# Optimization experiments

Measured on AMD Instinct MI355X. Metric: run time of the kernel, lower is better.

Reference implementation:

```python
import jax, jax.numpy as jnp
import numpy as np

N_ENTITY = 8000
N_REL = 100
N_GROUPS = 64
HIDDEN = 256
D_MODEL = 256
N_LAYERS = 2
N_HEADS = 4
GP = 64          # group_proj_dim
GH = 2           # group attn heads
D_TOTAL = D_MODEL * N_LAYERS
D_FEAT = D_TOTAL + 2 * HIDDEN
B, L = 16, 512


def time_enc(t, d):
    # sinusoidal temporal encoding: [..., d]
    i = jnp.arange(d // 2)
    freqs = jnp.exp(-jnp.log(10000.0) * (2.0 * i / d)).astype(t.dtype)
    ang = t[..., None] * freqs
    return jnp.concatenate([jnp.sin(ang), jnp.cos(ang)], axis=-1)


def layer_norm(x, w, b, eps=1e-5):
    mu = jnp.mean(x, axis=-1, keepdims=True)
    var = jnp.mean((x - mu) ** 2, axis=-1, keepdims=True)
    return (x - mu) / jnp.sqrt(var + eps) * w + b


def mh_attn(q, k, v, n_heads, mask=None):
    Bq, Lq, E = q.shape
    hd = E // n_heads
    qh = q.reshape(Bq, Lq, n_heads, hd)
    kh = k.reshape(Bq, -1, n_heads, hd)
    vh = v.reshape(Bq, -1, n_heads, hd)
    s = jnp.einsum('bqhd,bkhd->bhqk', qh, kh) / np.sqrt(hd).astype(np.float32)
    if mask is not None:
        s = jnp.where(mask, s, jnp.asarray(-1e9, s.dtype))
    a = jax.nn.softmax(s, axis=-1)
    return jnp.einsum('bhqk,bkhd->bqhd', a, vh).reshape(Bq, Lq, E)


def setup_inputs() -> dict:
    key = jax.random.key(0)
    ks = iter(jax.random.split(key, 48))
    w = lambda *s: jax.random.normal(next(ks), s, jnp.float32) * 0.02
    inp = {}
    inp['subs'] = jax.random.randint(next(ks), (B, L), 0, N_ENTITY)
    inp['marks'] = jax.random.randint(next(ks), (B, L), 0, N_REL)
    inp['objs'] = jax.random.randint(next(ks), (B, L), 0, N_ENTITY)
    inp['times'] = jax.random.uniform(next(ks), (B, L), jnp.float32)
    inp['dt'] = jax.random.uniform(next(ks), (B, L), jnp.float32)
    inp['mask'] = jax.random.randint(next(ks), (B, L), 0, 2).astype(bool)
    inp['group_map'] = jax.random.randint(next(ks), (N_ENTITY * N_REL,), 0, N_GROUPS)
    # AttNHP core params
    inp['obj_embed'] = w(N_ENTITY, D_MODEL)
    inp['core_Wq'] = w(N_LAYERS, D_MODEL, D_MODEL)
    inp['core_Wk'] = w(N_LAYERS, D_MODEL, D_MODEL)
    inp['core_Wv'] = w(N_LAYERS, D_MODEL, D_MODEL)
    inp['core_Wo'] = w(N_LAYERS, D_MODEL, D_MODEL)
    # GAttNHP params
    inp['sub_embed'] = w(N_ENTITY, HIDDEN)
    inp['rel_embed'] = w(N_REL, HIDDEN)
    inp['gp_w'] = w(D_FEAT, GP)
    inp['gp_b'] = jnp.zeros((GP,), jnp.float32)
    inp['ga_in_w'] = w(GP, 3 * GP)
    inp['ga_in_b'] = jnp.zeros((3 * GP,), jnp.float32)
    inp['ga_out_w'] = w(GP, GP)
    inp['ga_out_b'] = jnp.zeros((GP,), jnp.float32)
    inp['ffn_w1'] = w(GP, GP)
    inp['ffn_b1'] = jnp.zeros((GP,), jnp.float32)
    inp['ffn_w2'] = w(GP, GP)
    inp['ffn_b2'] = jnp.zeros((GP,), jnp.float32)
    inp['n1_w'] = jnp.ones((GP,), jnp.float32)
    inp['n1_b'] = jnp.zeros((GP,), jnp.float32)
    inp['n2_w'] = jnp.ones((GP,), jnp.float32)
    inp['n2_b'] = jnp.zeros((GP,), jnp.float32)
    inp['mg_w'] = w(D_FEAT + GP, D_FEAT)
    inp['mg_b'] = jnp.zeros((D_FEAT,), jnp.float32)
    inp['int_w'] = w(D_FEAT, N_ENTITY)
    inp['int_b'] = jnp.zeros((N_ENTITY,), jnp.float32)
    return inp


def reference(subs, marks, objs, times, dt, mask, group_map,
              obj_embed, core_Wq, core_Wk, core_Wv, core_Wo,
              sub_embed, rel_embed, gp_w, gp_b, ga_in_w, ga_in_b,
              ga_out_w, ga_out_b, ffn_w1, ffn_b1, ffn_w2, ffn_b2,
              n1_w, n1_b, n2_w, n2_b, mg_w, mg_b, int_w, int_b):
    Bb, Ll = objs.shape
    Lh = Ll - 1
    # ---- AttNHP core (forward_along_seqs) ----
    hist = objs[:, :-1]
    x = obj_embed[hist] + time_enc(times[:, :-1], D_MODEL) + time_enc(dt[:, :-1], D_MODEL)
    cur = time_enc(times[:, 1:], D_MODEL)                       # queries at query_times
    causal = jnp.tril(jnp.ones((Lh, Lh), bool))[None, None]     # [1,1,Lq,Lk]
    layer_outs = []
    for l in range(N_LAYERS):
        q = cur @ core_Wq[l]
        k = x @ core_Wk[l]
        v = x @ core_Wv[l]
        cur = cur + mh_attn(q, k, v, N_HEADS, causal) @ core_Wo[l]
        layer_outs.append(cur)
    enc_out = jnp.concatenate(layer_outs, axis=-1)              # [B,Lh,D_TOTAL]
    # ---- base features ----
    s_emb = jnp.broadcast_to(sub_embed[subs[:, 0]][:, None, :], (Bb, Lh, HIDDEN))
    r_emb = jnp.broadcast_to(rel_embed[marks[:, 0]][:, None, :], (Bb, Lh, HIDDEN))
    feats = jnp.concatenate([enc_out, s_emb, r_emb], axis=-1)   # [B,Lh,D_FEAT]
    # ---- group interaction: scatter-mean -> attn+ffn -> gather -> merge ----
    g_ids = group_map[subs * N_REL + marks][:, :-1]             # [B,Lh]
    flat_f = feats.reshape(-1, D_FEAT)
    fm = mask[:, :-1].reshape(-1).astype(flat_f.dtype)          # float validity mask
    keys = jnp.repeat(jnp.arange(Bb), Lh) * N_GROUPS + g_ids.reshape(-1)
    nseg = Bb * N_GROUPS
    gsum = jax.ops.segment_sum(flat_f * fm[:, None], keys, num_segments=nseg)
    gcnt = jax.ops.segment_sum(fm, keys, num_segments=nseg)
    rep = (gsum / jnp.maximum(gcnt, 1.0)[:, None]).reshape(Bb, N_GROUPS, D_FEAT)
    gp = rep @ gp_w + gp_b                                      # [B,G,64]
    qg, kg, vg = jnp.split(gp @ ga_in_w + ga_in_b, 3, axis=-1)
    ga = mh_attn(qg, kg, vg, GH) @ ga_out_w + ga_out_b
    gn = layer_norm(gp + ga, n1_w, n1_b)
    ff = jax.nn.relu(gn @ ffn_w1 + ffn_b1) @ ffn_w2 + ffn_b2
    gout = layer_norm(gn + ff, n2_w, n2_b)                      # [B,G,64]
    gathered = gout.reshape(-1, GP)[keys] * fm[:, None]         # zeros where invalid
    merged = jnp.concatenate([flat_f, gathered], axis=-1)
    enhanced = (merged @ mg_w + mg_b).reshape(Bb, Lh, D_FEAT)
    # ---- intensity head ----
    return jax.nn.softplus(enhanced @ int_w + int_b)            # [B,Lh,N_ENTITY]
```

## Files before the change

### kernel.cpp

```cpp
#include <hip/hip_runtime.h>
#include <hip/hip_bf16.h>
#include <cstdint>
#include <cstddef>

#define B_    16
#define L_    512
#define LH    511
#define RTOT  (B_*LH)
#define DM    256
#define DFEAT 1024
#define NG    64
#define GPDIM 64
#define NENT  8000
#define NRELS 100
#define RS    8000
#define RS2   16000

#define COL_X     0
#define COL_CUR   256
#define COL_Q     512
#define COL_K     768
#define COL_V     1024
#define COL_ATTN  1280
#define COL_FF    1536
#define COL_GATH  2560
#define COL_GSUM  3000
#define COL_GCNT  4100
#define COL_GP    4200
#define COL_GOUT  4300
#define COL_FLAG  5000
#define BCOL_ENCW 5248
#define BCOL_MGWT 11104
#define BCOL_MGA  12192
#define BCOL_WT   13824
#define BCOL_ENH  14848
#define N1        6912

#define WS_OFF_K  2228224ull
#define WS_OFF_V  (WS_OFF_K + 4186112ull)
#define WS_NEED2  (WS_OFF_V + 4194304ull)
#define WS2_BT    0ull
#define WS2_ENH   2359296ull
#define WS2_K     WS2_ENH
#define WS2_V     (WS2_K + 4186112ull)
#define WS_NEED3  (WS2_ENH + 16744448ull)

static constexpr float LN1E4_OVER_128 = 0.07195578415606394f;

typedef __attribute__((ext_vector_type(8))) short short8;
typedef __attribute__((ext_vector_type(4))) short sshort4;
typedef __attribute__((ext_vector_type(4))) float f32x4;
typedef __attribute__((ext_vector_type(2))) float f32x2;

__device__ __forceinline__ short bf16b(float x){
  union { __hip_bfloat16 h; short s; } u; u.h = __float2bfloat16(x); return u.s;
}

__device__ __forceinline__ float fast_softplus(float v) {
  return fmaxf(v, 0.f) + __logf(1.0f + __expf(-fabsf(v)));
}

__device__ __forceinline__ void gload16(const void* g, void* l) {
  __builtin_amdgcn_global_load_lds(
      (const __attribute__((address_space(1))) unsigned int*)g,
      (__attribute__((address_space(3))) unsigned int*)l, 16, 0, 0);
}

__global__ __launch_bounds__(256) void k_detect(const unsigned int* __restrict__ m,
                                                float* __restrict__ outbuf) {
  __shared__ int bad;
  if (threadIdx.x == 0) bad = 0;
  __syncthreads();
  int local = 0;
  for (int i = threadIdx.x; i < 2048; i += 256)
    if (m[i] > 1u) local = 1;
  if (local) bad = 1;
  __syncthreads();
  if (threadIdx.x == 0) ((int*)outbuf)[COL_FLAG] = bad;
}

__device__ __forceinline__ int mask_at(const void* m, int idx, int boolmode) {
  return boolmode ? (int)((const unsigned char*)m)[idx] : ((const int*)m)[idx];
}

__global__ __launch_bounds__(256) void k_build_x_cur(
    const int* __restrict__ objs, const float* __restrict__ times,
    const float* __restrict__ dts, const float* __restrict__ obj_embed,
    float* __restrict__ out)
{
  int bt = blockIdx.x;
  int b = bt / LH, t = bt - b * LH;
  int d = threadIdx.x;
  int i = d & 127;
  float freq = expf(-(float)i * LN1E4_OVER_128);
  float t0 = times[b*L_ + t];
  float t1 = times[b*L_ + t + 1];
  float dtv = dts[b*L_ + t];
  float a0 = t0*freq, ad = dtv*freq, a1 = t1*freq;
  bool lo = (d < 128);
  float te0 = lo ? sinf(a0) : cosf(a0);
  float ted = lo ? sinf(ad) : cosf(ad);
  float te1 = lo ? sinf(a1) : cosf(a1);
  int obj = objs[b*L_ + t];
  out[(size_t)bt*RS + COL_X   + d] = obj_embed[(size_t)obj*DM + d] + te0 + ted;
  out[(size_t)bt*RS + COL_CUR + d] = te1;
}

template<bool AF32, int EPI>
__global__ __launch_bounds__(256) void gemm_mfma(
    const void* __restrict__ Aptr, long strideA,
    const short* __restrict__ Bt, long strideB,
    const float* __restrict__ bias,
    float* __restrict__ Cf, long strideC,
    __hip_bfloat16* __restrict__ Cb, long strideCb,
    float* __restrict__ aux, long ldaux, int auxoff,
    int M, int K)
{
  int lane = threadIdx.x & 63;
  int wid  = threadIdx.x >> 6;
  int wm = wid >> 1, wn = wid & 1;
  int r15 = lane & 15, koct = lane >> 4;
  int m0 = blockIdx.y*128 + wm*64;
  int n0 = blockIdx.x*128 + wn*64;
  f32x4 acc[4][4] = {};
  int ar[4];
  #pragma unroll
  for (int mf = 0; mf < 4; ++mf) {
    int r = m0 + mf*16 + r15;
    ar[mf] = r < M ? r : M-1;
  }
  const short* Ab = (const short*)Aptr;
  const float* Af = (const float*)Aptr;
  for (int k0 = 0; k0 < K; k0 += 32) {
    int kk = k0 + koct*8;
    short8 a[4], b[4];
    #pragma unroll
    for (int mf = 0; mf < 4; ++mf) {
      if (AF32) {
        const float* p = Af + (size_t)ar[mf]*strideA + kk;
        f32x4 lo = *(const f32x4*)p;
        f32x4 hi = *(const f32x4*)(p + 4);
        short8 t;
        #pragma unroll
        for (int i = 0; i < 4; ++i) { t[i] = bf16b(lo[i]); t[i+4] = bf16b(hi[i]); }
        a[mf] = t;
      } else {
        a[mf] = *(const short8*)(Ab + (size_t)ar[mf]*strideA + kk);
      }
    }
    #pragma unroll
    for (int nf = 0; nf < 4; ++nf) {
      int n = n0 + nf*16 + r15;
      b[nf] = *(const short8*)(Bt + (size_t)n*strideB + kk);
    }
    #pragma unroll
    for (int mf = 0; mf < 4; ++mf)
      #pragma unroll
      for (int nf = 0; nf < 4; ++nf)
        acc[mf][nf] = __builtin_amdgcn_mfma_f32_16x16x32_bf16(a[mf], b[nf], acc[mf][nf], 0, 0, 0);
  }
  #pragma unroll
  for (int mf = 0; mf < 4; ++mf) {
    #pragma unroll
    for (int r = 0; r < 4; ++r) {
      int grow = m0 + mf*16 + koct*4 + r;
      if (grow >= M) continue;
      #pragma unroll
      for (int nf = 0; nf < 4; ++nf) {
        int gcol = n0 + nf*16 + r15;
        float v = acc[mf][nf][r];
        size_t ci = (size_t)grow*strideC + gcol;
        if (EPI == 2) {
          v += Cf[ci];
          Cf[ci] = v;
          aux[(size_t)grow*ldaux + auxoff + gcol] = v;
        } else {
          Cf[ci] = v;
        }
      }
    }
  }
}

template<int EPI>
__global__ __launch_bounds__(256) void gemm_mfma_lds(
    const short* __restrict__ A, long strideA,
    const short* __restrict__ Bt, long strideB,
    const float* __restrict__ bias,
    float* __restrict__ Cf, long strideC,
    __hip_bfloat16* __restrict__ Cb, long strideCb,
    __hip_bfloat16* __restrict__ Cb2, long strideCb2,
    int M, int N, int K)
{
  __shared__ short8 sA[128][8];
  __shared__ short8 sB[128][8];
  int tid = threadIdx.x;
  int lane = tid & 63;
  int w = tid >> 6;
  int wm = w >> 1, wn = w & 1;
  int r15 = lane & 15, koct = lane >> 4;

  int gx = gridDim.x;
  int nwg = gx * gridDim.y;
  int bid = blockIdx.y * gx + blockIdx.x;
  int bx, by;
  if (gridDim.y == 64 && (nwg & 7) == 0) {
    int xcd = bid & 7, c = bid >> 3;
    by = xcd*8 + (c & 7);
    bx = c >> 3;
  } else {
    bx = blockIdx.x; by = blockIdx.y;
  }
  int m0 = by * 128, n0 = bx * 128;

  const short* aSrc[4]; const short* bSrc[4];
  {
    int row = w*32 + (lane >> 3);
    int slot = lane & 7;
    #pragma unroll
    for (int c = 0; c < 4; ++c) {
      int r = row + c*8;
      int ga = m0 + r; if (ga > M-1) ga = M-1;
      int gb = n0 + r;
      int sw = slot ^ (r & 7);
      aSrc[c] = A  + (size_t)ga*strideA + sw*8;
      bSrc[c] = Bt + (size_t)gb*strideB + sw*8;
    }
  }

  f32x4 acc[4][4] = {};
  for (int k0 = 0; k0 < K; k0 += 64) {
    #pragma unroll
    for (int c = 0; c < 4; ++c) {
      gload16(aSrc[c] + k0, (short8*)sA + (w*4 + c)*64);
      gload16(bSrc[c] + k0, (short8*)sB + (w*4 + c)*64);
    }
    __syncthreads();
    #pragma unroll
    for (int ks = 0; ks < 2; ++ks) {
      short8 a[4], b[4];
      #pragma unroll
      for (int mf = 0; mf < 4; ++mf) {
        int lr = wm*64 + mf*16 + r15;
        a[mf] = sA[lr][(ks*4 + koct) ^ (lr & 7)];
      }
      #pragma unroll
      for (int nf = 0; nf < 4; ++nf) {
        int lr = wn*64 + nf*16 + r15;
        b[nf] = sB[lr][(ks*4 + koct) ^ (lr & 7)];
      }
      #pragma unroll
      for (int mf = 0; mf < 4; ++mf)
        #pragma unroll
        for (int nf = 0; nf < 4; ++nf)
          acc[mf][nf] = __builtin_amdgcn_mfma_f32_16x16x32_bf16(a[mf], b[nf], acc[mf][nf], 0, 0, 0);
    }
    __syncthreads();
  }
  #pragma unroll
  for (int mf = 0; mf < 4; ++mf) {
    #pragma unroll
    for (int r = 0; r < 4; ++r) {
      int grow = m0 + wm*64 + mf*16 + koct*4 + r;
      if (grow >= M) continue;
      #pragma unroll
      for (int nf = 0; nf < 4; ++nf) {
        int gcol = n0 + wn*64 + nf*16 + r15;
        if (gcol >= N) continue;
        float v = acc[mf][nf][r] + bias[gcol];
        if (EPI == 0) {
          __builtin_nontemporal_store(fast_softplus(v), &Cf[(size_t)grow*strideC + gcol]);
        } else {
          __hip_bfloat16 hb = __float2bfloat16(v);
          Cb[(size_t)grow*strideCb + gcol] = hb;
          if (Cb2) Cb2[(size_t)grow*strideCb2 + gcol] = hb;
        }
      }
    }
  }
}

__global__ __launch_bounds__(256) void k_transpose_bf16(
    const float* __restrict__ W, int ldw,
    __hip_bfloat16* __restrict__ Wt, long strideT)
{
  __shared__ float s[64][65];
  int n0 = blockIdx.x * 64, k0 = blockIdx.y * 64;
  int tid = threadIdx.x;
  for (int p = 0; p < 16; ++p) {
    int idx = p*256 + tid;
    int kk = idx >> 6, nn = idx & 63;
    s[kk][nn] = W[(size_t)(k0+kk)*ldw + n0 + nn];
  }
  __syncthreads();
  for (int p = 0; p < 16; ++p) {
    int idx = p*256 + tid;
    int nn = idx >> 6, kk = idx & 63;
    Wt[(size_t)(n0+nn)*strideT + k0 + kk] = __float2bfloat16(s[kk][nn]);
  }
}

__global__ __launch_bounds__(256) void k_castA(float* __restrict__ out)
{
  int r = blockIdx.x;
  int tid = threadIdx.x;
  const float* src = out + (size_t)r*RS + COL_FF;
  short* dst = (short*)out + (size_t)r*RS2 + BCOL_MGA;
  for (int i = tid; i < 1088; i += 256)
    dst[i] = bf16b(src[i]);
}

__global__ __launch_bounds__(256) void k_kvcast(
    const float* __restrict__ out, short* __restrict__ Kb, short* __restrict__ Vt)
{
  __shared__ float sV[32][65];
  int tt = blockIdx.x, bh = blockIdx.y;
  int b = bh >> 2, h = bh & 3;
  int tid = threadIdx.x;
  #pragma unroll
  for (int i = 0; i < 8; ++i) {
    int idx = i*256 + tid;
    int tp = idx >> 6, d = idx & 63;
    int t = tt*32 + tp;
    float vv = 0.f;
    if (t < LH) {
      const float* row = out + (size_t)(b*LH + t)*RS;
      Kb[((size_t)bh*511 + t)*64 + d] = bf16b(row[COL_K + h*64 + d]);
      vv = row[COL_V + h*64 + d];
    }
    sV[tp][d] = vv;
  }
  __syncthreads();
  #pragma unroll
  for (int i = 0; i < 8; ++i) {
    int idx = i*256 + tid;
    int d = idx >> 5, tp = idx & 31;
    Vt[((size_t)bh*64 + d)*512 + tt*32 + tp] = bf16b(sV[tp][d]);
  }
}

__global__ __launch_bounds__(64) void k_attn_mfma(float* __restrict__ out)
{
  int qt = blockIdx.x, h = blockIdx.y, b = blockIdx.z;
  int lane = threadIdx.x & 63;
  int r15 = lane & 15, koct = lane >> 4;
  __shared__ short Vt[64][40];
  __shared__ short Pl[16][40];
  const float* base = out + (size_t)b*LH*RS;

  int qrow = qt*16 + r15; if (qrow > LH-1) qrow = LH-1;
  const float* qp = base + (size_t)qrow*RS + COL_Q + h*64 + koct*8;
  short8 qf[2];
  #pragma unroll
  for (int d2 = 0; d2 < 2; ++d2) {
    f32x4 lo = *(const f32x4*)(qp + d2*32);
    f32x4 hi = *(const f32x4*)(qp + d2*32 + 4);
    short8 t;
    #pragma unroll
    for (int i = 0; i < 4; ++i) { t[i] = bf16b(lo[i]); t[i+4] = bf16b(hi[i]); }
    qf[d2] = t;
  }

  f32x4 o[4] = {};
  float m = -3.0e38f, l = 0.f;
  int qg = qt*16 + r15;
  int nt = qt/2 + 1;

  for (int ti = 0; ti < nt; ++ti) {
    int kv0 = ti*32;
    __syncthreads();
    {
      const float* vbase = base + COL_V + h*64 + lane;
      #pragma unroll 4
      for (int j = 0; j < 32; ++j) {
        int kvr = kv0 + j; if (kvr > LH-1) kvr = LH-1;
        Vt[lane][j] = bf16b(vbase[(size_t)kvr*RS]);
      }
    }
    f32x4 s[2] = {};
    #pragma unroll
    for (int kvf = 0; kvf < 2; ++kvf) {
      int kvr = kv0 + kvf*16 + r15; if (kvr > LH-1) kvr = LH-1;
      const float* kp = base + (size_t)kvr*RS + COL_K + h*64 + koct*8;
      #pragma unroll
      for (int d2 = 0; d2 < 2; ++d2) {
        f32x4 lo = *(const f32x4*)(kp + d2*32);
        f32x4 hi = *(const f32x4*)(kp + d2*32 + 4);
        short8 t;
        #pragma unroll
        for (int i = 0; i < 4; ++i) { t[i] = bf16b(lo[i]); t[i+4] = bf16b(hi[i]); }
        s[kvf] = __builtin_amdgcn_mfma_f32_16x16x32_bf16(t, qf[d2], s[kvf], 0, 0, 0);
      }
    }
    float sv[2][4];
    float mx = -3.0e38f;
    #pragma unroll
    for (int kvf = 0; kvf < 2; ++kvf)
      #pragma unroll
      for (int r = 0; r < 4; ++r) {
        int kvg = kv0 + kvf*16 + koct*4 + r;
        float x = s[kvf][r] * 0.125f;
        if (kvg > qg) x = -3.0e38f;
        sv[kvf][r] = x;
        mx = fmaxf(mx, x);
      }
    mx = fmaxf(mx, __shfl_xor(mx, 16));
    mx = fmaxf(mx, __shfl_xor(mx, 32));
    float mn = fmaxf(m, mx);
    float alpha = expf(m - mn);
    m = mn;
    float ls = 0.f;
    sshort4 pk[2];
    #pragma unroll
    for (int kvf = 0; kvf < 2; ++kvf)
      #pragma unroll
      for (int r = 0; r < 4; ++r) {
        float p = expf(sv[kvf][r] - mn);
        ls += p;
        pk[kvf][r] = bf16b(p);
      }
    l = l*alpha + ls;
    *(sshort4*)&Pl[r15][koct*4]      = pk[0];
    *(sshort4*)&Pl[r15][16 + koct*4] = pk[1];
    __syncthreads();
    float arr[4];
    #pragma unroll
    for (int r = 0; r < 4; ++r) arr[r] = __shfl(alpha, koct*4 + r);
    #pragma unroll
    for (int df = 0; df < 4; ++df)
      #pragma unroll
      for (int r = 0; r < 4; ++r) o[df][r] *= arr[r];
    short8 pa = *(const short8*)&Pl[r15][koct*8];
    #pragma unroll
    for (int df = 0; df < 4; ++df) {
      short8 vb = *(const short8*)&Vt[df*16 + r15][koct*8];
      o[df] = __builtin_amdgcn_mfma_f32_16x16x32_bf16(pa, vb, o[df], 0, 0, 0);
    }
  }
  l += __shfl_xor(l, 16);
  l += __shfl_xor(l, 32);
  float linv = 1.f / l;
  float lr[4];
  #pragma unroll
  for (int r = 0; r < 4; ++r) lr[r] = __shfl(linv, koct*4 + r);
  #pragma unroll
  for (int df = 0; df < 4; ++df)
    #pragma unroll
    for (int r = 0; r < 4; ++r) {
      int qq = qt*16 + koct*4 + r;
      if (qq < LH)
        out[((size_t)(b*LH + qq))*RS + COL_ATTN + h*64 + df*16 + r15] = o[df][r] * lr[r];
    }
}

__global__ __launch_bounds__(64) void k_attn_mfma2(
    const short* __restrict__ Kb, const short* __restrict__ Vt,
    float* __restrict__ out)
{
  int qt = blockIdx.x, h = blockIdx.y, b = blockIdx.z;
  int lane = threadIdx.x & 63;
  int r15 = lane & 15, koct = lane >> 4;
  __shared__ short Pl[16][40];
  int bh = b*4 + h;
  const short* Kbh = Kb + (size_t)bh*511*64;
  const short* Vbh = Vt + (size_t)bh*64*512;
  const float* base = out + (size_t)b*LH*RS;

  int qrow = qt*16 + r15; if (qrow > LH-1) qrow = LH-1;
  const float* qp = base + (size_t)qrow*RS + COL_Q + h*64 + koct*8;
  short8 qf[2];
  #pragma unroll
  for (int d2 = 0; d2 < 2; ++d2) {
    f32x4 lo = *(const f32x4*)(qp + d2*32);
    f32x4 hi = *(const f32x4*)(qp + d2*32 + 4);
    short8 t;
    #pragma unroll
    for (int i = 0; i < 4; ++i) { t[i] = bf16b(lo[i]); t[i+4] = bf16b(hi[i]); }
    qf[d2] = t;
  }

  f32x4 o[4] = {};
  float m = -3.0e38f, l = 0.f;
  int qg = qt*16 + r15;
  int nt = qt/2 + 1;

  for (int ti = 0; ti < nt; ++ti) {
    int kv0 = ti*32;
    f32x4 s[2] = {};
    #pragma unroll
    for (int kvf = 0; kvf < 2; ++kvf) {
      int kvr = kv0 + kvf*16 + r15; if (kvr > LH-1) kvr = LH-1;
      const short* kp = Kbh + (size_t)kvr*64 + koct*8;
      short8 ka0 = *(const short8*)kp;
      short8 ka1 = *(const short8*)(kp + 32);
      s[kvf] = __builtin_amdgcn_mfma_f32_16x16x32_bf16(ka0, qf[0], s[kvf], 0, 0, 0);
      s[kvf] = __builtin_amdgcn_mfma_f32_16x16x32_bf16(ka1, qf[1], s[kvf], 0, 0, 0);
    }
    float sv[2][4];
    float mx = -3.0e38f;
    #pragma unroll
    for (int kvf = 0; kvf < 2; ++kvf)
      #pragma unroll
      for (int r = 0; r < 4; ++r) {
        int kvg = kv0 + kvf*16 + koct*4 + r;
        float x = s[kvf][r] * 0.125f;
        if (kvg > qg) x = -3.0e38f;
        sv[kvf][r] = x;
        mx = fmaxf(mx, x);
      }
    mx = fmaxf(mx, __shfl_xor(mx, 16));
    mx = fmaxf(mx, __shfl_xor(mx, 32));
    float mn = fmaxf(m, mx);
    float alpha = expf(m - mn);
    m = mn;
    float ls = 0.f;
    sshort4 pk[2];
    #pragma unroll
    for (int kvf = 0; kvf < 2; ++kvf)
      #pragma unroll
      for (int r = 0; r < 4; ++r) {
        float p = expf(sv[kvf][r] - mn);
        ls += p;
        pk[kvf][r] = bf16b(p);
      }
    l = l*alpha + ls;
    *(sshort4*)&Pl[r15][koct*4]      = pk[0];
    *(sshort4*)&Pl[r15][16 + koct*4] = pk[1];
    __syncthreads();
    float arr[4];
    #pragma unroll
    for (int r = 0; r < 4; ++r) arr[r] = __shfl(alpha, koct*4 + r);
    #pragma unroll
    for (int df = 0; df < 4; ++df)
      #pragma unroll
      for (int r = 0; r < 4; ++r) o[df][r] *= arr[r];
    short8 pa = *(const short8*)&Pl[r15][koct*8];
    #pragma unroll
    for (int df = 0; df < 4; ++df) {
      short8 vb = *(const short8*)(Vbh + (size_t)(df*16 + r15)*512 + kv0 + koct*8);
      o[df] = __builtin_amdgcn_mfma_f32_16x16x32_bf16(pa, vb, o[df], 0, 0, 0);
    }
  }
  l += __shfl_xor(l, 16);
  l += __shfl_xor(l, 32);
  float linv = 1.f / l;
  float lr[4];
  #pragma unroll
  for (int r = 0; r < 4; ++r) lr[r] = __shfl(linv, koct*4 + r);
  #pragma unroll
  for (int df = 0; df < 4; ++df)
    #pragma unroll
    for (int r = 0; r < 4; ++r) {
      int qq = qt*16 + koct*4 + r;
      if (qq < LH)
        out[((size_t)(b*LH + qq))*RS + COL_ATTN + h*64 + df*16 + r15] = o[df][r] * lr[r];
    }
}

__global__ __launch_bounds__(256) void k_feats(
    const int* __restrict__ subs, const int* __restrict__ marks,
    const float* __restrict__ sub_embed, const float* __restrict__ rel_embed,
    float* __restrict__ out)
{
  int bt = blockIdx.x;
  int b = bt / LH;
  int d = threadIdx.x;
  out[(size_t)bt*RS + COL_FF + 512 + d] = sub_embed[(size_t)subs[b*L_]*256 + d];
  out[(size_t)bt*RS + COL_FF + 768 + d] = rel_embed[(size_t)marks[b*L_]*256 + d];
}

__global__ __launch_bounds__(256) void k_zero(float* __restrict__ out)
{
  int s = blockIdx.x;
  for (int c = threadIdx.x; c < DFEAT; c += 256)
    out[(size_t)s*RS + COL_GSUM + c] = 0.f;
  if (threadIdx.x == 0) out[(size_t)s*RS + COL_GCNT] = 0.f;
}

__global__ __launch_bounds__(256) void k_segsum(
    const int* __restrict__ subs, const int* __restrict__ marks,
    const void* __restrict__ mask,
    const int* __restrict__ group_map, float* __restrict__ out)
{
  int bt = blockIdx.x;
  int b = bt / LH, t = bt - b*LH;
  int boolmode = ((const int*)out)[COL_FLAG];
  if (!mask_at(mask, b*L_ + t, boolmode)) return;
  int gid = group_map[subs[b*L_+t]*NRELS + marks[b*L_+t]];
  int key = b*NG + gid;
  const float* src = out + (size_t)bt*RS + COL_FF;
  float* dst = out + (size_t)key*RS + COL_GSUM;
  for (int d = threadIdx.x; d < DFEAT; d += 256)
    atomicAdd(&dst[d], src[d]);
  if (threadIdx.x == 0) atomicAdd(&out[(size_t)key*RS + COL_GCNT], 1.0f);
}

__global__ __launch_bounds__(64) void k_gp(
    const float* __restrict__ gp_w, const float* __restrict__ gp_b,
    float* __restrict__ out)
{
  int s = blockIdx.x;
  int j = threadIdx.x;
  float inv = 1.0f / fmaxf(out[(size_t)s*RS + COL_GCNT], 1.0f);
  float acc = 0.f;
  const float* gs = out + (size_t)s*RS + COL_GSUM;
  for (int k2 = 0; k2 < DFEAT; ++k2)
    acc += gs[k2] * gp_w[k2*GPDIM + j];
  out[(size_t)s*RS + COL_GP + j] = acc * inv + gp_b[j];
}

__global__ __launch_bounds__(256) void k_group(
    const float* __restrict__ ga_in_w, const float* __restrict__ ga_in_b,
    const float* __restrict__ ga_out_w, const float* __restrict__ ga_out_b,
    const float* __restrict__ ffn_w1, const float* __restrict__ ffn_b1,
    const float* __restrict__ ffn_w2, const float* __restrict__ ffn_b2,
    const float* __restrict__ n1_w, const float* __restrict__ n1_b,
    const float* __restrict__ n2_w, const float* __restrict__ n2_b,
    float* __restrict__ out)
{
  __shared__ float sGP[64][64];
  __shared__ float sQ[64][64];
  __shared__ float sK[64][64];
  __shared__ float sV[64][64];
  int b = blockIdx.x, tid = threadIdx.x;
  for (int i = tid; i < 4096; i += 256)
    sGP[i>>6][i&63] = out[(size_t)(b*64 + (i>>6))*RS + COL_GP + (i&63)];
  __syncthreads();
  for (int i = tid; i < 64*192; i += 256) {
    int g = i / 192, c = i - g*192;
    float acc = ga_in_b[c];
    for (int k2 = 0; k2 < 64; ++k2) acc += sGP[g][k2] * ga_in_w[k2*192 + c];
    if (c < 64)       sQ[g][c]      = acc;
    else if (c < 128) sK[g][c-64]   = acc;
    else              sV[g][c-128]  = acc;
  }
  __syncthreads();
  if (tid < 128) {
    int qi = tid >> 1, h = tid & 1, base = h*32;
    float sc[64];
    float mx = -3.0e38f;
    #pragma unroll
    for (int k2 = 0; k2 < 64; ++k2) {
      float d2 = 0.f;
      #pragma unroll
      for (int d = 0; d < 32; ++d) d2 += sQ[qi][base+d] * sK[k2][base+d];
      d2 *= 0.17677669529663689f;
      sc[k2] = d2;
      mx = fmaxf(mx, d2);
    }
    float den = 0.f;
    #pragma unroll
    for (int k2 = 0; k2 < 64; ++k2) { sc[k2] = expf(sc[k2]-mx); den += sc[k2]; }
    float inv = 1.f/den;
    #pragma unroll
    for (int d = 0; d < 32; ++d) {
      float acc = 0.f;
      #pragma unroll
      for (int k2 = 0; k2 < 64; ++k2) acc += sc[k2] * sV[k2][base+d];
      sQ[qi][base+d] = acc * inv;
    }
  }
  __syncthreads();
  for (int i = tid; i < 4096; i += 256) {
    int g = i>>6, c = i&63;
    float acc = ga_out_b[c];
    for (int k2 = 0; k2 < 64; ++k2) acc += sQ[g][k2] * ga_out_w[k2*64 + c];
    sK[g][c] = sGP[g][c] + acc;
  }
  __syncthreads();
  if (tid < 64) {
    int g = tid;
    float mu = 0.f; for (int c=0;c<64;c++) mu += sK[g][c]; mu *= (1.f/64.f);
    float var = 0.f; for (int c=0;c<64;c++){float d2=sK[g][c]-mu; var += d2*d2;} var *= (1.f/64.f);
    float inv = 1.0f / sqrtf(var + 1e-5f);
    for (int c=0;c<64;c++) sK[g][c] = (sK[g][c]-mu)*inv*n1_w[c] + n1_b[c];
  }
  __syncthreads();
  for (int i = tid; i < 4096; i += 256) {
    int g = i>>6, c = i&63;
    float acc = ffn_b1[c];
    for (int k2 = 0; k2 < 64; ++k2) acc += sK[g][k2] * ffn_w1[k2*64 + c];
    sV[g][c] = fmaxf(acc, 0.f);
  }
  __syncthreads();
  for (int i = tid; i < 4096; i += 256) {
    int g = i>>6, c = i&63;
    float acc = ffn_b2[c];
    for (int k2 = 0; k2 < 64; ++k2) acc += sV[g][k2] * ffn_w2[k2*64 + c];
    sGP[g][c] = sK[g][c] + acc;
  }
  __syncthreads();
  if (tid < 64) {
    int g = tid;
    float mu = 0.f; for (int c=0;c<64;c++) mu += sGP[g][c]; mu *= (1.f/64.f);
    float var = 0.f; for (int c=0;c<64;c++){float d2=sGP[g][c]-mu; var += d2*d2;} var *= (1.f/64.f);
    float inv = 1.0f / sqrtf(var + 1e-5f);
    for (int c=0;c<64;c++)
      out[(size_t)(b*64 + g)*RS + COL_GOUT + c] = (sGP[g][c]-mu)*inv*n2_w[c] + n2_b[c];
  }
}

__global__ __launch_bounds__(64) void k_gather(
    const int* __restrict__ subs, const int* __restrict__ marks,
    const void* __restrict__ mask,
    const int* __restrict__ group_map, float* __restrict__ out)
{
  int bt = blockIdx.x;
  int b = bt / LH, t = bt - b*LH;
  int j = threadIdx.x;
  int boolmode = ((const int*)out)[COL_FLAG];
  float val = 0.f;
  if (mask_at(mask, b*L_ + t, boolmode)) {
    int gid = group_map[subs[b*L_+t]*NRELS + marks[b*L_+t]];
    val = out[(size_t)(b*NG + gid)*RS + COL_GOUT + j];
  }
  out[(size_t)bt*RS + COL_GATH + j] = val;
}

__global__ __launch_bounds__(256) void k_tail_v6(
    const float* __restrict__ int_w, const float* __restrict__ int_b,
    float* __restrict__ out)
{
  __shared__ short8 sA[16][128];
  __shared__ short8 sB[2][128][8];
  int m0 = blockIdx.x * 16;
  int tid = threadIdx.x;
  int lane = tid & 63;
  int w = tid >> 6;
  int r15 = lane & 15, koct = lane >> 4;
  const short* eb = (const short*)out + BCOL_ENH;

  for (int idx = tid; idx < 16*128; idx += 256) {
    int r = idx >> 7, c8 = idx & 127;
    int row = m0 + r; if (row > RTOT-1) row = RTOT-1;
    sA[r][c8 ^ (r & 7)] = *(const short8*)(eb + (size_t)row*RS2 + c8*8);
  }

  int tn2 = tid & 63;
  int tk4 = tid >> 6;
  int xA = r15 & 7;

  f32x2 v[16];
  auto issueB = [&](int s) {
    int ntile = s >> 4, ks = s & 15;
    int nb = N1 + ntile*128 + tn2*2;
    int ncl = nb <= NENT-2 ? nb : NENT-2;
    const float* bp = int_w + (size_t)(ks*64 + tk4*16)*NENT + ncl;
    #pragma unroll
    for (int i = 0; i < 16; ++i) v[i] = *(const f32x2*)(bp + (size_t)i*NENT);
  };

  issueB(0);
  __syncthreads();

  f32x4 acc[2] = {};
  for (int s = 0; s < 144; ++s) {
    int ks = s & 15;
    int buf = s & 1;
    {
      short h0[16], h1[16];
      #pragma unroll
      for (int i = 0; i < 16; ++i) { h0[i] = bf16b(v[i][0]); h1[i] = bf16b(v[i][1]); }
      short8 p0lo, p0hi, p1lo, p1hi;
      #pragma unroll
      for (int i = 0; i < 8; ++i) {
        p0lo[i] = h0[i]; p0hi[i] = h0[i+8];
        p1lo[i] = h1[i]; p1hi[i] = h1[i+8];
      }
      int nl0 = tn2*2, nl1 = tn2*2 + 1;
      sB[buf][nl0][(tk4*2 + 0) ^ (nl0 & 7)] = p0lo;
      sB[buf][nl0][(tk4*2 + 1) ^ (nl0 & 7)] = p0hi;
      sB[buf][nl1][(tk4*2 + 0) ^ (nl1 & 7)] = p1lo;
      sB[buf][nl1][(tk4*2 + 1) ^ (nl1 & 7)] = p1hi;
    }
    if (s + 1 < 144) issueB(s + 1);
    __syncthreads();
    #pragma unroll
    for (int ksub = 0; ksub < 2; ++ksub) {
      int c8A = ks*8 + ksub*4 + koct;
      short8 a0 = sA[r15][c8A ^ xA];
      #pragma unroll
      for (int nf = 0; nf < 2; ++nf) {
        int nloc = w*32 + nf*16 + r15;
        short8 b = sB[buf][nloc][(ksub*4 + koct) ^ (nloc & 7)];
        acc[nf] = __builtin_amdgcn_mfma_f32_16x16x32_bf16(a0, b, acc[nf], 0, 0, 0);
      }
    }
    if (ks == 15) {
      int n0 = N1 + (s >> 4)*128;
      #pragma unroll
      for (int nf = 0; nf < 2; ++nf) {
        int n = n0 + w*32 + nf*16 + r15;
        if (n < NENT) {
          float bv = int_b[n];
          #pragma unroll
          for (int r = 0; r < 4; ++r) {
            int g = m0 + koct*4 + r;
            if (g < RTOT)
              __builtin_nontemporal_store(fast_softplus(acc[nf][r] + bv),
                                          &out[(size_t)g*RS + n]);
          }
        }
        acc[nf] = (f32x4){0.f, 0.f, 0.f, 0.f};
      }
    }
  }
}

__global__ __launch_bounds__(256) void k_tail_v8(
    const short* __restrict__ Bt, const float* __restrict__ int_b,
    float* __restrict__ out)
{
  __shared__ short8 sA[16][128];
  __shared__ short8 sB[2][128][8];
  int m0 = blockIdx.x * 16;
  int tid = threadIdx.x;
  int lane = tid & 63;
  int w = tid >> 6;
  int r15 = lane & 15, koct = lane >> 4;
  const short* eb = (const short*)out + BCOL_ENH;

  for (int idx = tid; idx < 16*128; idx += 256) {
    int r = idx >> 7, c8 = idx & 127;
    int row = m0 + r; if (row > RTOT-1) row = RTOT-1;
    sA[r][c8 ^ (r & 7)] = *(const short8*)(eb + (size_t)row*RS2 + c8*8);
  }

  int rl8 = w*8 + (lane >> 3);
  int slot = lane & 7;
  int xA = r15 & 7;

  auto issueB = [&](int s) {
    int ntile = s >> 4, ks = s & 15;
    #pragma unroll
    for (int c = 0; c < 4; ++c) {
      int rowL = c*32 + rl8;
      int wsrow = ntile*128 + rowL;
      if (wsrow > 1087) wsrow = 1087;
      int sw = slot ^ (rowL & 7);
      gload16(Bt + (size_t)wsrow*1024 + ks*64 + sw*8,
              (short8*)&sB[s & 1][c*32 + w*8][0]);
    }
  };

  issueB(0);
  __syncthreads();

  f32x4 acc[2] = {};
  for (int s = 0; s < 144; ++s) {
    int ks = s & 15, buf = s & 1;
    if (s + 1 < 144) issueB(s + 1);
    #pragma unroll
    for (int ksub = 0; ksub < 2; ++ksub) {
      int c8A = ks*8 + ksub*4 + koct;
      short8 a0 = sA[r15][c8A ^ xA];
      #pragma unroll
      for (int nf = 0; nf < 2; ++nf) {
        int nloc = w*32 + nf*16 + r15;
        short8 b = sB[buf][nloc][(ksub*4 + koct) ^ (nloc & 7)];
        acc[nf] = __builtin_amdgcn_mfma_f32_16x16x32_bf16(a0, b, acc[nf], 0, 0, 0);
      }
    }
    if (ks == 15) {
      int n0 = N1 + (s >> 4)*128;
      #pragma unroll
      for (int nf = 0; nf < 2; ++nf) {
        int n = n0 + w*32 + nf*16 + r15;
        if (n < NENT) {
          float bv = int_b[n];
          #pragma unroll
          for (int r = 0; r < 4; ++r) {
            int g = m0 + koct*4 + r;
            if (g < RTOT)
              __builtin_nontemporal_store(fast_softplus(acc[nf][r] + bv),
                                          &out[(size_t)g*RS + n]);
          }
        }
        acc[nf] = (f32x4){0.f, 0.f, 0.f, 0.f};
      }
    }
    __syncthreads();
  }
}

extern "C" void kernel_launch(void* const* d_in, const int* in_sizes, int n_in,
                              void* d_out, int out_size, void* d_ws, size_t ws_size,
                              hipStream_t stream)
{
  const int*   subs      = (const int*)  d_in[0];
  const int*   marks     = (const int*)  d_in[1];
  const int*   objs      = (const int*)  d_in[2];
  const float* times     = (const float*)d_in[3];
  const float* dts       = (const float*)d_in[4];
  const void*  mask      =               d_in[5];
  const int*   group_map = (const int*)  d_in[6];
  const float* obj_embed = (const float*)d_in[7];
  const float* Wq        = (const float*)d_in[8];
  const float* Wk        = (const float*)d_in[9];
  const float* Wv        = (const float*)d_in[10];
  const float* Wo        = (const float*)d_in[11];
  const float* sub_embed = (const float*)d_in[12];
  const float* rel_embed = (const float*)d_in[13];
  const float* gp_w      = (const float*)d_in[14];
  const float* gp_b      = (const float*)d_in[15];
  const float* ga_in_w   = (const float*)d_in[16];
  const float* ga_in_b   = (const float*)d_in[17];
  const float* ga_out_w  = (const float*)d_in[18];
  const float* ga_out_b  = (const float*)d_in[19];
  const float* ffn_w1    = (const float*)d_in[20];
  const float* ffn_b1    = (const float*)d_in[21];
  const float* ffn_w2    = (const float*)d_in[22];
  const float* ffn_b2    = (const float*)d_in[23];
  const float* n1_w      = (const float*)d_in[24];
  const float* n1_b      = (const float*)d_in[25];
  const float* n2_w      = (const float*)d_in[26];
  const float* n2_b      = (const float*)d_in[27];
  const float* mg_w      = (const float*)d_in[28];
  const float* mg_b      = (const float*)d_in[29];
  const float* int_w     = (const float*)d_in[30];
  const float* int_b     = (const float*)d_in[31];
  float* out = (float*)d_out;
  __hip_bfloat16* ob = (__hip_bfloat16*)d_out;

  bool ws_ok  = ws_size >= (size_t)1088 * 1024 * sizeof(__hip_bfloat16);
  bool ws_ok2 = ws_size >= WS_NEED2;
  bool ws_ok3 = ws_size >= WS_NEED3;

  short* wsK = ws_ok3 ? (short*)((char*)d_ws + WS2_K) : (short*)((char*)d_ws + WS_OFF_K);
  short* wsV = ws_ok3 ? (short*)((char*)d_ws + WS2_V) : (short*)((char*)d_ws + WS_OFF_V);
  __hip_bfloat16* wsENH = (__hip_bfloat16*)((char*)d_ws + WS2_ENH);

  k_detect<<<1, 256, 0, stream>>>((const unsigned int*)mask, out);
  k_transpose_bf16<<<dim3(N1/64, DFEAT/64), 256, 0, stream>>>(int_w, NENT, ob + BCOL_WT, RS2);
  k_transpose_bf16<<<dim3(DFEAT/64, 1088/64), 256, 0, stream>>>(mg_w, DFEAT, ob + BCOL_MGWT, RS2);
  if (ws_ok) {
    k_transpose_bf16<<<dim3(1088/64, DFEAT/64), 256, 0, stream>>>(
        int_w + N1, NENT, (__hip_bfloat16*)d_ws, 1024);
  }
  for (int l = 0; l < 2; ++l) {
    const float* ws[4] = { Wq + (size_t)l*DM*DM, Wk + (size_t)l*DM*DM,
                           Wv + (size_t)l*DM*DM, Wo + (size_t)l*DM*DM };
    for (int j = 0; j < 4; ++j)
      k_transpose_bf16<<<dim3(4, 4), 256, 0, stream>>>(
          ws[j], DM, ob + BCOL_ENCW + (size_t)((l*4 + j)*256)*RS2, RS2);
  }

  k_build_x_cur<<<RTOT, 256, 0, stream>>>(objs, times, dts, obj_embed, out);

  for (int l = 0; l < 2; ++l) {
    const short* encw = (const short*)(ob + BCOL_ENCW);
    const short* wtq = encw + (size_t)((l*4 + 0)*256)*RS2;
    const short* wtk = encw + (size_t)((l*4 + 1)*256)*RS2;
    const short* wto = encw + (size_t)((l*4 + 3)*256)*RS2;
    gemm_mfma<true, 3><<<dim3(2, 64), 256, 0, stream>>>(
        out + COL_CUR, RS, wtq, RS2, nullptr,
        out + COL_Q, RS, nullptr, 0, nullptr, 0, 0, RTOT, DM);
    gemm_mfma<true, 3><<<dim3(4, 64), 256, 0, stream>>>(
        out + COL_X, RS, wtk, RS2, nullptr,
        out + COL_K, RS, nullptr, 0, nullptr, 0, 0, RTOT, DM);
    if (ws_ok2) {
      k_kvcast<<<dim3(16, 64), 256, 0, stream>>>(out, wsK, wsV);
      k_attn_mfma2<<<dim3(32, 4, B_), 64, 0, stream>>>(wsK, wsV, out);
    } else {
      k_attn_mfma<<<dim3(32, 4, B_), 64, 0, stream>>>(out);
    }
    gemm_mfma<true, 2><<<dim3(2, 64), 256, 0, stream>>>(
        out + COL_ATTN, RS, wto, RS2, nullptr,
        out + COL_CUR, RS, nullptr, 0, out + COL_FF, RS, l*DM, RTOT, DM);
  }

  k_feats<<<RTOT, 256, 0, stream>>>(subs, marks, sub_embed, rel_embed, out);
  k_zero<<<1024, 256, 0, stream>>>(out);
  k_segsum<<<RTOT, 256, 0, stream>>>(subs, marks, mask, group_map, out);
  k_gp<<<1024, 64, 0, stream>>>(gp_w, gp_b, out);
  k_group<<<B_, 256, 0, stream>>>(ga_in_w, ga_in_b, ga_out_w, ga_out_b,
                                  ffn_w1, ffn_b1, ffn_w2, ffn_b2,
                                  n1_w, n1_b, n2_w, n2_b, out);
  k_gather<<<RTOT, 64, 0, stream>>>(subs, marks, mask, group_map, out);

  k_castA<<<RTOT, 256, 0, stream>>>(out);
  if (ws_ok3) {
    gemm_mfma_lds<1><<<dim3(DFEAT/128, 64), 256, 0, stream>>>(
        (const short*)(ob + BCOL_MGA), RS2, (const short*)(ob + BCOL_MGWT), RS2, mg_b,
        nullptr, 0, wsENH, 1024, nullptr, 0, RTOT, DFEAT, 1088);
    gemm_mfma_lds<0><<<dim3(N1/128, (RTOT+127)/128), 256, 0, stream>>>(
        (const short*)wsENH, 1024, (const short*)(ob + BCOL_WT), RS2, int_b,
        out, RS, nullptr, 0, nullptr, 0, RTOT, N1, DFEAT);
    gemm_mfma_lds<0><<<dim3(9, 64), 256, 0, stream>>>(
        (const short*)wsENH, 1024, (const short*)d_ws, 1024, int_b + N1,
        out + N1, RS, nullptr, 0, nullptr, 0, RTOT, 1088, DFEAT);
  } else {
    gemm_mfma_lds<1><<<dim3(DFEAT/128, 64), 256, 0, stream>>>(
        (const short*)(ob + BCOL_MGA), RS2, (const short*)(ob + BCOL_MGWT), RS2, mg_b,
        nullptr, 0, ob + BCOL_ENH, RS2, nullptr, 0, RTOT, DFEAT, 1088);
    gemm_mfma_lds<0><<<dim3(N1/128, (RTOT+127)/128), 256, 0, stream>>>(
        (const short*)(ob + BCOL_ENH), RS2, (const short*)(ob + BCOL_WT), RS2, int_b,
        out, RS, nullptr, 0, nullptr, 0, RTOT, N1, DFEAT);
    if (ws_ok)
      k_tail_v8<<<RTOT/16, 256, 0, stream>>>((const short*)d_ws, int_b, out);
    else
      k_tail_v6<<<RTOT/16, 256, 0, stream>>>(int_w, int_b, out);
  }
}
```

Baseline: 656.1 us.

## Replace atomic segment-sum with per-group gather reduction; fuse gather with bf16 cast

The zero, atomic segment-sum and group-projection kernels become one kernel with one block per (batch, group). Each block scans the sequence for matching tokens, sums their features in registers, and applies the 1024x64 projection from shared memory. This removes float atomics and three launches, but each block rereads the mask and group ids for all 511 tokens and loops serially over them. The group-output gather is also fused with the bf16 cast of the merge input, dropping another launch and a pass over the gathered column.

New measurement: 639.0 us. -2.6%, faster.

```diff
diff --git a/kernel.cpp b/kernel.cpp
--- a/kernel.cpp
+++ b/kernel.cpp
@@ -23,9 +23,6 @@
 #define COL_V     1024
 #define COL_ATTN  1280
 #define COL_FF    1536
-#define COL_GATH  2560
-#define COL_GSUM  3000
-#define COL_GCNT  4100
 #define COL_GP    4200
 #define COL_GOUT  4300
 #define COL_FLAG  5000
@@ -300,16 +297,6 @@
   }
 }
 
-__global__ __launch_bounds__(256) void k_castA(float* __restrict__ out)
-{
-  int r = blockIdx.x;
-  int tid = threadIdx.x;
-  const float* src = out + (size_t)r*RS + COL_FF;
-  short* dst = (short*)out + (size_t)r*RS2 + BCOL_MGA;
-  for (int i = tid; i < 1088; i += 256)
-    dst[i] = bf16b(src[i]);
-}
-
 __global__ __launch_bounds__(256) void k_kvcast(
     const float* __restrict__ out, short* __restrict__ Kb, short* __restrict__ Vt)
 {
@@ -569,44 +556,58 @@
   out[(size_t)bt*RS + COL_FF + 768 + d] = rel_embed[(size_t)marks[b*L_]*256 + d];
 }
 
-__global__ __launch_bounds__(256) void k_zero(float* __restrict__ out)
-{
-  int s = blockIdx.x;
-  for (int c = threadIdx.x; c < DFEAT; c += 256)
-    out[(size_t)s*RS + COL_GSUM + c] = 0.f;
-  if (threadIdx.x == 0) out[(size_t)s*RS + COL_GCNT] = 0.f;
-}
-
-__global__ __launch_bounds__(256) void k_segsum(
+__global__ __launch_bounds__(256) void k_seg2(
     const int* __restrict__ subs, const int* __restrict__ marks,
-    const void* __restrict__ mask,
-    const int* __restrict__ group_map, float* __restrict__ out)
-{
-  int bt = blockIdx.x;
-  int b = bt / LH, t = bt - b*LH;
-  int boolmode = ((const int*)out)[COL_FLAG];
-  if (!mask_at(mask, b*L_ + t, boolmode)) return;
-  int gid = group_map[subs[b*L_+t]*NRELS + marks[b*L_+t]];
-  int key = b*NG + gid;
-  const float* src = out + (size_t)bt*RS + COL_FF;
-  float* dst = out + (size_t)key*RS + COL_GSUM;
-  for (int d = threadIdx.x; d < DFEAT; d += 256)
-    atomicAdd(&dst[d], src[d]);
-  if (threadIdx.x == 0) atomicAdd(&out[(size_t)key*RS + COL_GCNT], 1.0f);
-}
-
-__global__ __launch_bounds__(64) void k_gp(
+    const void* __restrict__ mask, const int* __restrict__ group_map,
     const float* __restrict__ gp_w, const float* __restrict__ gp_b,
     float* __restrict__ out)
 {
-  int s = blockIdx.x;
-  int j = threadIdx.x;
-  float inv = 1.0f / fmaxf(out[(size_t)s*RS + COL_GCNT], 1.0f);
-  float acc = 0.f;
-  const float* gs = out + (size_t)s*RS + COL_GSUM;
-  for (int k2 = 0; k2 < DFEAT; ++k2)
-    acc += gs[k2] * gp_w[k2*GPDIM + j];
-  out[(size_t)s*RS + COL_GP + j] = acc * inv + gp_b[j];
+  __shared__ unsigned char match[512];
+  __shared__ float macc[1024];
+  __shared__ float pacc[4][64];
+  __shared__ int cnt;
+  int key = blockIdx.x;
+  int b = key >> 6, g = key & 63;
+  int tid = threadIdx.x;
+  int boolmode = ((const int*)out)[COL_FLAG];
+  if (tid == 0) cnt = 0;
+  __syncthreads();
+  int lc = 0;
+  for (int t = tid; t < LH; t += 256) {
+    int mt = 0;
+    if (mask_at(mask, b*L_ + t, boolmode)) {
+      int gid = group_map[subs[b*L_ + t]*NRELS + marks[b*L_ + t]];
+      mt = (gid == g) ? 1 : 0;
+    }
+    match[t] = (unsigned char)mt;
+    lc += mt;
+  }
+  if (lc) atomicAdd(&cnt, lc);
+  __syncthreads();
+
+  f32x4 acc = {0.f, 0.f, 0.f, 0.f};
+  int c0 = tid * 4;
+  for (int t = 0; t < LH; ++t) {
+    if (match[t]) {
+      f32x4 v = *(const f32x4*)(out + (size_t)(b*LH + t)*RS + COL_FF + c0);
+      acc.x += v.x; acc.y += v.y; acc.z += v.z; acc.w += v.w;
+    }
+  }
+  *(f32x4*)&macc[c0] = acc;
+  __syncthreads();
+
+  int j = tid & 63, ch = tid >> 6;
+  float p = 0.f;
+  int kb = ch * 256;
+  for (int k2 = kb; k2 < kb + 256; ++k2)
+    p += macc[k2] * gp_w[k2*GPDIM + j];
+  pacc[ch][j] = p;
+  __syncthreads();
+  if (tid < 64) {
+    float inv = 1.0f / fmaxf((float)cnt, 1.0f);
+    float s = pacc[0][tid] + pacc[1][tid] + pacc[2][tid] + pacc[3][tid];
+    out[(size_t)key*RS + COL_GP + tid] = s * inv + gp_b[tid];
+  }
 }
 
 __global__ __launch_bounds__(256) void k_group(
@@ -700,21 +701,29 @@
   }
 }
 
-__global__ __launch_bounds__(64) void k_gather(
+__global__ __launch_bounds__(256) void k_gather_cast(
     const int* __restrict__ subs, const int* __restrict__ marks,
-    const void* __restrict__ mask,
-    const int* __restrict__ group_map, float* __restrict__ out)
-{
+    const void* __restrict__ mask, const int* __restrict__ group_map,
+    float* __restrict__ out)
+{
+  __shared__ float gv[64];
   int bt = blockIdx.x;
   int b = bt / LH, t = bt - b*LH;
-  int j = threadIdx.x;
+  int tid = threadIdx.x;
   int boolmode = ((const int*)out)[COL_FLAG];
-  float val = 0.f;
-  if (mask_at(mask, b*L_ + t, boolmode)) {
-    int gid = group_map[subs[b*L_+t]*NRELS + marks[b*L_+t]];
-    val = out[(size_t)(b*NG + gid)*RS + COL_GOUT + j];
-  }
-  out[(size_t)bt*RS + COL_GATH + j] = val;
+  if (tid < 64) {
+    float val = 0.f;
+    if (mask_at(mask, b*L_ + t, boolmode)) {
+      int gid = group_map[subs[b*L_+t]*NRELS + marks[b*L_+t]];
+      val = out[(size_t)(b*NG + gid)*RS + COL_GOUT + tid];
+    }
+    gv[tid] = val;
+  }
+  __syncthreads();
+  const float* src = out + (size_t)bt*RS + COL_FF;
+  short* dst = (short*)out + (size_t)bt*RS2 + BCOL_MGA;
+  for (int i = tid; i < 1088; i += 256)
+    dst[i] = bf16b(i < 1024 ? src[i] : gv[i - 1024]);
 }
 
 __global__ __launch_bounds__(256) void k_tail_v6(
@@ -970,15 +979,12 @@
   }
 
   k_feats<<<RTOT, 256, 0, stream>>>(subs, marks, sub_embed, rel_embed, out);
-  k_zero<<<1024, 256, 0, stream>>>(out);
-  k_segsum<<<RTOT, 256, 0, stream>>>(subs, marks, mask, group_map, out);
-  k_gp<<<1024, 64, 0, stream>>>(gp_w, gp_b, out);
+  k_seg2<<<1024, 256, 0, stream>>>(subs, marks, mask, group_map, gp_w, gp_b, out);
   k_group<<<B_, 256, 0, stream>>>(ga_in_w, ga_in_b, ga_out_w, ga_out_b,
                                   ffn_w1, ffn_b1, ffn_w2, ffn_b2,
                                   n1_w, n1_b, n2_w, n2_b, out);
-  k_gather<<<RTOT, 64, 0, stream>>>(subs, marks, mask, group_map, out);
-
-  k_castA<<<RTOT, 256, 0, stream>>>(out);
+  k_gather_cast<<<RTOT, 256, 0, stream>>>(subs, marks, mask, group_map, out);
+
   if (ws_ok3) {
     gemm_mfma_lds<1><<<dim3(DFEAT/128, 64), 256, 0, stream>>>(
         (const short*)(ob + BCOL_MGA), RS2, (const short*)(ob + BCOL_MGWT), RS2, mg_b,
```
